# Kernel tuning notes

Hardware: AMD Instinct MI355X
Metric: run time of the kernel (lower is better)

Reference implementation:

```python
import jax, jax.numpy as jnp
import numpy as np


def gcn_conv(x, edge_index, edge_weight, W, b):
    """Faithful PyG GCNConv: add self-loops (weight 1), symmetric normalization,
    linear transform, weighted sum aggregation at target nodes, then bias."""
    N = x.shape[0]
    loops = jnp.arange(N, dtype=edge_index.dtype)
    row = jnp.concatenate([edge_index[0], loops])  # source j
    col = jnp.concatenate([edge_index[1], loops])  # target i
    ew = jnp.concatenate([edge_weight, jnp.ones((N,), dtype=edge_weight.dtype)])
    deg = jax.ops.segment_sum(ew, col, num_segments=N)  # [N]
    dinv = jnp.where(deg > 0, jax.lax.rsqrt(deg), 0.0)
    norm = dinv[row] * ew * dinv[col]  # [E+N]
    xw = x @ W  # [N, F_out]
    msgs = xw[row] * norm[:, None]  # [E+N, F_out]
    out = jax.ops.segment_sum(msgs, col, num_segments=N)  # [N, F_out]
    return out + b


def setup_inputs() -> dict:
    key = jax.random.key(0)
    k = jax.random.split(key, 8)
    N, E, Fin, Fhid, Fout = 50000, 800000, 128, 128, 64
    x = jax.random.normal(k[0], (N, Fin), dtype=jnp.float32)
    edge_index = jax.random.randint(k[1], (2, E), 0, N, dtype=jnp.int64)
    edge_weight = jax.random.uniform(k[2], (E,), dtype=jnp.float32)
    s0 = 1.0 / np.sqrt(Fin)
    s1 = 1.0 / np.sqrt(Fhid)
    W0 = jax.random.uniform(k[3], (Fin, Fhid), jnp.float32, -s0, s0)
    b0 = jnp.zeros((Fhid,), jnp.float32)
    W1 = jax.random.uniform(k[4], (Fhid, Fout), jnp.float32, -s1, s1)
    b1 = jnp.zeros((Fout,), jnp.float32)
    return {"x": x, "edge_index": edge_index, "edge_weight": edge_weight,
            "W0": W0, "b0": b0, "W1": W1, "b1": b1}


def reference(x, edge_index, edge_weight, W0, b0, W1, b1):
    # Encoder with num_layers=2, drop_p=0.0 (identity), activation=ReLU
    h = gcn_conv(x, edge_index, edge_weight, W0, b0)
    h = jax.nn.relu(h)
    h = gcn_conv(h, edge_index, edge_weight, W1, b1)
    h = jax.nn.relu(h)
    return h
```

## Files before the change

### kernel.cpp

```cpp
#include <hip/hip_runtime.h>

#define MAXDEG 48
#define BSH 6
#define BNODES 64
#define BCAP 2048

typedef unsigned short ushort_t;
typedef __attribute__((ext_vector_type(8))) short short8;
typedef __attribute__((ext_vector_type(4))) float f32x4;

__device__ inline ushort_t f2bf(float f) {
    union { float f; unsigned u; } v;
    v.f = f;
    unsigned r = v.u + 0x7fff + ((v.u >> 16) & 1);
    return (ushort_t)(r >> 16);
}

__device__ inline float bf2f_lo(unsigned u) {
    union { unsigned u; float f; } v;
    v.u = u << 16;
    return v.f;
}

__device__ inline float bf2f_hi(unsigned u) {
    union { unsigned u; float f; } v;
    v.u = u & 0xffff0000u;
    return v.f;
}


__global__ void k_setup(const float* __restrict__ W0, ushort_t* __restrict__ wp0,
                        const float* __restrict__ W1, ushort_t* __restrict__ wp1,
                        int* __restrict__ bcur, int NB) {
    int tid = blockIdx.x * blockDim.x + threadIdx.x;
    int stride = gridDim.x * blockDim.x;
    for (int i = tid; i < NB; i += stride) bcur[i] = 0;
    for (int e = tid; e < 16384; e += stride) {
        int j = e & 7, l = (e >> 3) & 63, ct = e >> 9;
        int t = ct & 7, c = ct >> 3;
        int k = 32 * c + (l >> 4) * 8 + j;
        int n = 16 * t + (l & 15);
        wp0[e] = f2bf(W0[k * 128 + n]);
    }
    for (int e = tid; e < 8192; e += stride) {
        int j = e & 7, l = (e >> 3) & 63, ct = e >> 9;
        int t = ct & 3, c = ct >> 2;
        int k = 32 * c + (l >> 4) * 8 + j;
        int n = 16 * t + (l & 15);
        wp1[e] = f2bf(W1[k * 64 + n]);
    }
}


__global__ __launch_bounds__(256) void k_scatter(const int* __restrict__ row,
                                                 const int* __restrict__ col,
                                                 const float* __restrict__ ew,
                                                 int* __restrict__ bcur,
                                                 uint2* __restrict__ recs, int E, int NB) {
    __shared__ int cnt[1024];
    __shared__ int base[1024];
    const int t = threadIdx.x;
    const size_t e0 = (size_t)blockIdx.x * 1024;
    for (int i = t; i < NB; i += 256) cnt[i] = 0;
    __syncthreads();
    int ck[4], rk[4];
#pragma unroll
    for (int j = 0; j < 4; ++j) {
        size_t e = e0 + (size_t)j * 256 + t;
        ck[j] = -1;
        if (e < (size_t)E) {
            int c = col[e];
            ck[j] = c;
            rk[j] = atomicAdd(&cnt[c >> BSH], 1);
        }
    }
    __syncthreads();
    for (int i = t; i < NB; i += 256) {
        int c = cnt[i];
        base[i] = c ? atomicAdd(&bcur[i], c) : 0;
    }
    __syncthreads();
#pragma unroll
    for (int j = 0; j < 4; ++j) {
        if (ck[j] >= 0) {
            size_t e = e0 + (size_t)j * 256 + t;
            int c = ck[j];
            int b = c >> BSH;
            int idx = base[b] + rk[j];
            if (idx < BCAP) {
                uint2 r;
                r.x = (unsigned)row[e] | ((unsigned)(c & (BNODES - 1)) << 16);
                r.y = __float_as_uint(ew[e]);
                recs[(size_t)b * BCAP + idx] = r;
            }
        }
    }
}


__global__ __launch_bounds__(256) void k_ell_build(const uint2* __restrict__ recs,
                                                   const int* __restrict__ bcur,
                                                   uint2* __restrict__ ell,
                                                   int* __restrict__ counts,
                                                   float* __restrict__ dinv, int N) {
    __shared__ uint2 tile[BNODES * MAXDEG];
    __shared__ int cnt[BNODES];
    const int b = blockIdx.x;
    const int t = threadIdx.x;
    if (t < BNODES) cnt[t] = 0;
    __syncthreads();
    const size_t s = (size_t)b * BCAP;
    const int ne = min(bcur[b], BCAP);
    for (int i = t; i < ne; i += 256) {
        uint2 r = recs[s + i];
        int dl = (r.x >> 16) & (BNODES - 1);
        int pos = atomicAdd(&cnt[dl], 1);
        if (pos < MAXDEG) {
            uint2 c;
            c.x = r.x & 0xffffu;
            c.y = r.y;
            tile[dl * MAXDEG + pos] = c;
        }
    }
    __syncthreads();
    const int node0 = b << BSH;
    if (t < BNODES) {
        int node = node0 + t;
        if (node < N) {
            int cn = min(cnt[t], MAXDEG);
            float sum = 1.0f;
            for (int j = 0; j < cn; ++j) sum += __uint_as_float(tile[t * MAXDEG + j].y);
            dinv[node] = rsqrtf(sum);
            counts[node] = cn;
        }
    }
    __syncthreads();
    const int nvalid = min(BNODES, N - node0);
    const int total = nvalid * MAXDEG;
    for (int i = t; i < total; i += 256) {
        int nl = i / MAXDEG;
        int slot = i - nl * MAXDEG;
        if (slot < min(cnt[nl], MAXDEG))
            ell[(size_t)node0 * MAXDEG + i] = tile[i];
    }
}


__global__ __launch_bounds__(256) void k_gemm1(const float* __restrict__ X,
                                               const uint4* __restrict__ Wp,
                                               ushort_t* __restrict__ Y, int N) {
    const int wave = threadIdx.x >> 6;
    const int lane = threadIdx.x & 63;
    const int m0 = blockIdx.x * 64 + wave * 16;
    if (m0 >= N) return;
    const int q = lane >> 4;
    const int mr = lane & 15;
    const int rowc = min(m0 + mr, N - 1);

    short8 a[4];
    const float* xr = X + (size_t)rowc * 128 + q * 8;
#pragma unroll
    for (int c = 0; c < 4; ++c) {
        float4 v0 = *(const float4*)(xr + 32 * c);
        float4 v1 = *(const float4*)(xr + 32 * c + 4);
        a[c][0] = (short)f2bf(v0.x); a[c][1] = (short)f2bf(v0.y);
        a[c][2] = (short)f2bf(v0.z); a[c][3] = (short)f2bf(v0.w);
        a[c][4] = (short)f2bf(v1.x); a[c][5] = (short)f2bf(v1.y);
        a[c][6] = (short)f2bf(v1.z); a[c][7] = (short)f2bf(v1.w);
    }

#pragma unroll
    for (int t = 0; t < 8; ++t) {
        f32x4 acc = {0.0f, 0.0f, 0.0f, 0.0f};
#pragma unroll
        for (int c = 0; c < 4; ++c) {
            uint4 bw = Wp[(size_t)(c * 8 + t) * 64 + lane];
            short8 b;
            __builtin_memcpy(&b, &bw, 16);
            acc = __builtin_amdgcn_mfma_f32_16x16x32_bf16(a[c], b, acc, 0, 0, 0);
        }
        const int colbase = 16 * t + mr;
#pragma unroll
        for (int r = 0; r < 4; ++r) {
            int orow = m0 + q * 4 + r;
            if (orow < N) Y[(size_t)orow * 128 + colbase] = f2bf(acc[r]);
        }
    }
}


__global__ __launch_bounds__(256) void k_gather128_gemm2(
        const int* __restrict__ counts, const uint2* __restrict__ ell,
        const float* __restrict__ dinv, const unsigned* __restrict__ xwb,
        const float* __restrict__ b0, const uint4* __restrict__ wp1,
        ushort_t* __restrict__ xw2b, int N) {
    __shared__ ushort_t h1[16][136];
    const int wave = threadIdx.x >> 6, lane = threadIdx.x & 63;
    const int node0 = blockIdx.x * 16;

#pragma unroll
    for (int k = 0; k < 4; ++k) {
        const int nl = wave * 4 + k;
        const int node = node0 + nl;
        unsigned packed = 0u;
        if (node < N) {
            float di = dinv[node];
            int cnt = min(counts[node], MAXDEG);
            int sv = 0;
            float wv = 0.0f;
            if (lane < cnt) {
                uint2 rec = ell[(size_t)node * MAXDEG + lane];
                sv = (int)rec.x;
                wv = dinv[sv] * __uint_as_float(rec.y) * di;
            }
            unsigned u0 = xwb[(size_t)node * 64 + lane];
            float2 bb = ((const float2*)b0)[lane];
            float sw = di * di;
            float ax = bb.x + bf2f_lo(u0) * sw;
            float ay = bb.y + bf2f_hi(u0) * sw;
            int j = 0;
            for (; j + 4 <= cnt; j += 4) {
                int s0 = __shfl(sv, j), s1 = __shfl(sv, j + 1),
                    s2 = __shfl(sv, j + 2), s3 = __shfl(sv, j + 3);
                float w0 = __shfl(wv, j), w1 = __shfl(wv, j + 1),
                      w2 = __shfl(wv, j + 2), w3 = __shfl(wv, j + 3);
                unsigned v0 = xwb[(size_t)s0 * 64 + lane];
                unsigned v1 = xwb[(size_t)s1 * 64 + lane];
                unsigned v2 = xwb[(size_t)s2 * 64 + lane];
                unsigned v3 = xwb[(size_t)s3 * 64 + lane];
                ax += bf2f_lo(v0) * w0; ay += bf2f_hi(v0) * w0;
                ax += bf2f_lo(v1) * w1; ay += bf2f_hi(v1) * w1;
                ax += bf2f_lo(v2) * w2; ay += bf2f_hi(v2) * w2;
                ax += bf2f_lo(v3) * w3; ay += bf2f_hi(v3) * w3;
            }
            for (; j < cnt; ++j) {
                int s = __shfl(sv, j);
                float w = __shfl(wv, j);
                unsigned v = xwb[(size_t)s * 64 + lane];
                ax += bf2f_lo(v) * w; ay += bf2f_hi(v) * w;
            }
            packed = ((unsigned)f2bf(fmaxf(ay, 0.0f)) << 16) | f2bf(fmaxf(ax, 0.0f));
        }
        *(unsigned*)&h1[nl][2 * lane] = packed;
    }
    __syncthreads();

    const int q = lane >> 4, mr = lane & 15;
    short8 a[4];
#pragma unroll
    for (int c = 0; c < 4; ++c)
        __builtin_memcpy(&a[c], &h1[mr][32 * c + 8 * q], 16);
    f32x4 acc = {0.0f, 0.0f, 0.0f, 0.0f};
#pragma unroll
    for (int c = 0; c < 4; ++c) {
        uint4 bw = wp1[(size_t)(c * 4 + wave) * 64 + lane];
        short8 bf;
        __builtin_memcpy(&bf, &bw, 16);
        acc = __builtin_amdgcn_mfma_f32_16x16x32_bf16(a[c], bf, acc, 0, 0, 0);
    }
    const int colb = 16 * wave + mr;
#pragma unroll
    for (int r = 0; r < 4; ++r) {
        int orow = node0 + q * 4 + r;
        if (orow < N) xw2b[(size_t)orow * 64 + colb] = f2bf(acc[r]);
    }
}


__global__ __launch_bounds__(256) void k_gather64_relu(const int* __restrict__ counts,
                                                       const uint2* __restrict__ ell,
                                                       const float* __restrict__ dinv,
                                                       const ushort_t* __restrict__ xwb,
                                                       const float* __restrict__ bias,
                                                       float* __restrict__ h, int N) {
    int node = (blockIdx.x * 256 + threadIdx.x) >> 6;
    int lane = threadIdx.x & 63;
    if (node >= N) return;
    float di = dinv[node];
    int cnt = min(counts[node], MAXDEG);

    int sv = 0;
    float wv = 0.0f;
    if (lane < cnt) {
        uint2 rec = ell[(size_t)node * MAXDEG + lane];
        sv = (int)rec.x;
        wv = dinv[sv] * __uint_as_float(rec.y) * di;
    }

    float acc = bias[lane] + bf2f_lo((unsigned)xwb[(size_t)node * 64 + lane]) * di * di;

    int j = 0;
    for (; j + 4 <= cnt; j += 4) {
        int s0 = __shfl(sv, j), s1 = __shfl(sv, j + 1), s2 = __shfl(sv, j + 2), s3 = __shfl(sv, j + 3);
        float w0 = __shfl(wv, j), w1 = __shfl(wv, j + 1), w2 = __shfl(wv, j + 2), w3 = __shfl(wv, j + 3);
        float v0 = bf2f_lo((unsigned)xwb[(size_t)s0 * 64 + lane]);
        float v1 = bf2f_lo((unsigned)xwb[(size_t)s1 * 64 + lane]);
        float v2 = bf2f_lo((unsigned)xwb[(size_t)s2 * 64 + lane]);
        float v3 = bf2f_lo((unsigned)xwb[(size_t)s3 * 64 + lane]);
        acc += v0 * w0 + v1 * w1 + v2 * w2 + v3 * w3;
    }
    for (; j < cnt; ++j) {
        acc += bf2f_lo((unsigned)xwb[(size_t)__shfl(sv, j) * 64 + lane]) * __shfl(wv, j);
    }
    h[(size_t)node * 64 + lane] = fmaxf(acc, 0.0f);
}


extern "C" void kernel_launch(void* const* d_in, const int* in_sizes, int n_in,
                              void* d_out, int out_size, void* d_ws, size_t ws_size,
                              hipStream_t stream) {
    const float* x  = (const float*)d_in[0];
    const int*   ei = (const int*)d_in[1];
    const float* ew = (const float*)d_in[2];
    const float* W0 = (const float*)d_in[3];
    const float* b0 = (const float*)d_in[4];
    const float* W1 = (const float*)d_in[5];
    const float* b1 = (const float*)d_in[6];
    float* out = (float*)d_out;

    const int Fhid = in_sizes[4];
    const int Fin  = in_sizes[3] / Fhid;
    const int N    = in_sizes[0] / Fin;
    const int E    = in_sizes[2];
    const int NB   = (N + BNODES - 1) >> BSH;

    const int* row = ei;
    const int* col = ei + E;

    char* w = (char*)d_ws;
    auto alloc = [&](size_t bytes) {
        char* p = w;
        w += (bytes + 255) & ~(size_t)255;
        return p;
    };
    float*    dinv   = (float*)alloc((size_t)N * 4);
    int*      counts = (int*)alloc((size_t)N * 4);
    int*      bcur   = (int*)alloc((size_t)NB * 4);
    uint2*    recs   = (uint2*)alloc((size_t)NB * BCAP * 8);
    uint2*    ell    = (uint2*)alloc((size_t)N * MAXDEG * 8);
    ushort_t* xw1b   = (ushort_t*)alloc((size_t)N * 128 * 2);
    ushort_t* xw2b   = (ushort_t*)alloc((size_t)N * 64 * 2);
    ushort_t* wp0    = (ushort_t*)alloc(16384 * 2);
    ushort_t* wp1    = (ushort_t*)alloc(8192 * 2);

    const int T = 256;
    const int GB = (N + 63) / 64;

    k_setup<<<32, T, 0, stream>>>(W0, wp0, W1, wp1, bcur, NB);
    k_scatter<<<(E + 1023) / 1024, T, 0, stream>>>(row, col, ew, bcur, recs, E, NB);
    k_ell_build<<<NB, T, 0, stream>>>(recs, bcur, ell, counts, dinv, N);
    k_gemm1<<<GB, T, 0, stream>>>(x, (const uint4*)wp0, xw1b, N);
    k_gather128_gemm2<<<(N + 15) / 16, T, 0, stream>>>(counts, ell, dinv,
                                                       (const unsigned*)xw1b, b0,
                                                       (const uint4*)wp1, xw2b, N);
    k_gather64_relu<<<(N + 3) / 4, T, 0, stream>>>(counts, ell, dinv, xw2b, b1, out, N);
}
```

Before: 200.6 us.

## Build ELL with direct global atomics and fuse scatter with first GEMM

Replaces the two-pass bucketed scatter plus ELL build with a single pass that places each edge directly into the ELL slot using per-node global atomics, accumulating degree with float atomics. The dinv normalization is computed lazily via rsqrt of the degree inside the gather kernels. The scatter blocks are interleaved with the first GEMM blocks in one launch so both run concurrently. The gather128+GEMM2 kernel now handles 4 nodes per block for more parallelism, but wastes three quarters of its MFMA rows. Nondeterministic edge order and float atomic ordering change the rounding of results.

```diff
diff --git a/kernel.cpp b/kernel.cpp
--- a/kernel.cpp
+++ b/kernel.cpp
@@ -1,9 +1,6 @@
 #include <hip/hip_runtime.h>
 
 #define MAXDEG 48
-#define BSH 6
-#define BNODES 64
-#define BCAP 2048
 
 typedef unsigned short ushort_t;
 typedef __attribute__((ext_vector_type(8))) short short8;
@@ -29,12 +26,18 @@
 }
 
 
-__global__ void k_setup(const float* __restrict__ W0, ushort_t* __restrict__ wp0,
-                        const float* __restrict__ W1, ushort_t* __restrict__ wp1,
-                        int* __restrict__ bcur, int NB) {
+__global__ __launch_bounds__(256) void k_setup(const float* __restrict__ W0,
+                                               ushort_t* __restrict__ wp0,
+                                               const float* __restrict__ W1,
+                                               ushort_t* __restrict__ wp1,
+                                               int* __restrict__ counts,
+                                               float* __restrict__ deg, int N) {
     int tid = blockIdx.x * blockDim.x + threadIdx.x;
     int stride = gridDim.x * blockDim.x;
-    for (int i = tid; i < NB; i += stride) bcur[i] = 0;
+    for (int i = tid; i < N; i += stride) {
+        counts[i] = 0;
+        deg[i] = 0.0f;
+    }
     for (int e = tid; e < 16384; e += stride) {
         int j = e & 7, l = (e >> 3) & 63, ct = e >> 9;
         int t = ct & 7, c = ct >> 3;
@@ -52,106 +55,12 @@
 }
 
 
-__global__ __launch_bounds__(256) void k_scatter(const int* __restrict__ row,
-                                                 const int* __restrict__ col,
-                                                 const float* __restrict__ ew,
-                                                 int* __restrict__ bcur,
-                                                 uint2* __restrict__ recs, int E, int NB) {
-    __shared__ int cnt[1024];
-    __shared__ int base[1024];
-    const int t = threadIdx.x;
-    const size_t e0 = (size_t)blockIdx.x * 1024;
-    for (int i = t; i < NB; i += 256) cnt[i] = 0;
-    __syncthreads();
-    int ck[4], rk[4];
-#pragma unroll
-    for (int j = 0; j < 4; ++j) {
-        size_t e = e0 + (size_t)j * 256 + t;
-        ck[j] = -1;
-        if (e < (size_t)E) {
-            int c = col[e];
-            ck[j] = c;
-            rk[j] = atomicAdd(&cnt[c >> BSH], 1);
-        }
-    }
-    __syncthreads();
-    for (int i = t; i < NB; i += 256) {
-        int c = cnt[i];
-        base[i] = c ? atomicAdd(&bcur[i], c) : 0;
-    }
-    __syncthreads();
-#pragma unroll
-    for (int j = 0; j < 4; ++j) {
-        if (ck[j] >= 0) {
-            size_t e = e0 + (size_t)j * 256 + t;
-            int c = ck[j];
-            int b = c >> BSH;
-            int idx = base[b] + rk[j];
-            if (idx < BCAP) {
-                uint2 r;
-                r.x = (unsigned)row[e] | ((unsigned)(c & (BNODES - 1)) << 16);
-                r.y = __float_as_uint(ew[e]);
-                recs[(size_t)b * BCAP + idx] = r;
-            }
-        }
-    }
-}
-
-
-__global__ __launch_bounds__(256) void k_ell_build(const uint2* __restrict__ recs,
-                                                   const int* __restrict__ bcur,
-                                                   uint2* __restrict__ ell,
-                                                   int* __restrict__ counts,
-                                                   float* __restrict__ dinv, int N) {
-    __shared__ uint2 tile[BNODES * MAXDEG];
-    __shared__ int cnt[BNODES];
-    const int b = blockIdx.x;
-    const int t = threadIdx.x;
-    if (t < BNODES) cnt[t] = 0;
-    __syncthreads();
-    const size_t s = (size_t)b * BCAP;
-    const int ne = min(bcur[b], BCAP);
-    for (int i = t; i < ne; i += 256) {
-        uint2 r = recs[s + i];
-        int dl = (r.x >> 16) & (BNODES - 1);
-        int pos = atomicAdd(&cnt[dl], 1);
-        if (pos < MAXDEG) {
-            uint2 c;
-            c.x = r.x & 0xffffu;
-            c.y = r.y;
-            tile[dl * MAXDEG + pos] = c;
-        }
-    }
-    __syncthreads();
-    const int node0 = b << BSH;
-    if (t < BNODES) {
-        int node = node0 + t;
-        if (node < N) {
-            int cn = min(cnt[t], MAXDEG);
-            float sum = 1.0f;
-            for (int j = 0; j < cn; ++j) sum += __uint_as_float(tile[t * MAXDEG + j].y);
-            dinv[node] = rsqrtf(sum);
-            counts[node] = cn;
-        }
-    }
-    __syncthreads();
-    const int nvalid = min(BNODES, N - node0);
-    const int total = nvalid * MAXDEG;
-    for (int i = t; i < total; i += 256) {
-        int nl = i / MAXDEG;
-        int slot = i - nl * MAXDEG;
-        if (slot < min(cnt[nl], MAXDEG))
-            ell[(size_t)node0 * MAXDEG + i] = tile[i];
-    }
-}
-
-
-__global__ __launch_bounds__(256) void k_gemm1(const float* __restrict__ X,
-                                               const uint4* __restrict__ Wp,
-                                               ushort_t* __restrict__ Y, int N) {
+__device__ inline void gemm1_body(const float* __restrict__ X,
+                                  const uint4* __restrict__ Wp,
+                                  ushort_t* __restrict__ Y, int N, int g) {
     const int wave = threadIdx.x >> 6;
     const int lane = threadIdx.x & 63;
-    const int m0 = blockIdx.x * 64 + wave * 16;
+    const int m0 = g * 64 + wave * 16;
     if (m0 >= N) return;
     const int q = lane >> 4;
     const int mr = lane & 15;
@@ -189,67 +98,105 @@
 }
 
 
+__global__ __launch_bounds__(256) void k_scatter_gemm1(
+        const int* __restrict__ row, const int* __restrict__ col,
+        const float* __restrict__ ew, int* __restrict__ counts,
+        float* __restrict__ deg, uint2* __restrict__ ell, int E,
+        const float* __restrict__ x, const uint4* __restrict__ wp0,
+        ushort_t* __restrict__ xw1b, int N, int GB, int SB) {
+    const int bid = blockIdx.x;
+    const int npair = 2 * min(GB, SB);
+    bool isg;
+    int sub;
+    if (bid < npair) {
+        isg = (bid & 1) == 0;
+        sub = bid >> 1;
+    } else {
+        sub = min(GB, SB) + (bid - npair);
+        isg = GB > SB;
+    }
+    if (isg) {
+        gemm1_body(x, wp0, xw1b, N, sub);
+        return;
+    }
+    const int t = threadIdx.x;
+    const size_t e0 = (size_t)sub * 1024;
+#pragma unroll
+    for (int j = 0; j < 4; ++j) {
+        size_t e = e0 + (size_t)j * 256 + t;
+        if (e < (size_t)E) {
+            int c = col[e];
+            float w = ew[e];
+            int pos = atomicAdd(&counts[c], 1);
+            atomicAdd(&deg[c], w);
+            if (pos < MAXDEG) {
+                uint2 r;
+                r.x = (unsigned)row[e];
+                r.y = __float_as_uint(w);
+                ell[(size_t)c * MAXDEG + pos] = r;
+            }
+        }
+    }
+}
+
+
 __global__ __launch_bounds__(256) void k_gather128_gemm2(
         const int* __restrict__ counts, const uint2* __restrict__ ell,
-        const float* __restrict__ dinv, const unsigned* __restrict__ xwb,
+        const float* __restrict__ deg, const unsigned* __restrict__ xwb,
         const float* __restrict__ b0, const uint4* __restrict__ wp1,
         ushort_t* __restrict__ xw2b, int N) {
-    __shared__ ushort_t h1[16][136];
+    __shared__ ushort_t h1[4][136];
     const int wave = threadIdx.x >> 6, lane = threadIdx.x & 63;
-    const int node0 = blockIdx.x * 16;
-
-#pragma unroll
-    for (int k = 0; k < 4; ++k) {
-        const int nl = wave * 4 + k;
-        const int node = node0 + nl;
-        unsigned packed = 0u;
-        if (node < N) {
-            float di = dinv[node];
-            int cnt = min(counts[node], MAXDEG);
-            int sv = 0;
-            float wv = 0.0f;
-            if (lane < cnt) {
-                uint2 rec = ell[(size_t)node * MAXDEG + lane];
-                sv = (int)rec.x;
-                wv = dinv[sv] * __uint_as_float(rec.y) * di;
-            }
-            unsigned u0 = xwb[(size_t)node * 64 + lane];
-            float2 bb = ((const float2*)b0)[lane];
-            float sw = di * di;
-            float ax = bb.x + bf2f_lo(u0) * sw;
-            float ay = bb.y + bf2f_hi(u0) * sw;
-            int j = 0;
-            for (; j + 4 <= cnt; j += 4) {
-                int s0 = __shfl(sv, j), s1 = __shfl(sv, j + 1),
-                    s2 = __shfl(sv, j + 2), s3 = __shfl(sv, j + 3);
-                float w0 = __shfl(wv, j), w1 = __shfl(wv, j + 1),
-                      w2 = __shfl(wv, j + 2), w3 = __shfl(wv, j + 3);
-                unsigned v0 = xwb[(size_t)s0 * 64 + lane];
-                unsigned v1 = xwb[(size_t)s1 * 64 + lane];
-                unsigned v2 = xwb[(size_t)s2 * 64 + lane];
-                unsigned v3 = xwb[(size_t)s3 * 64 + lane];
-                ax += bf2f_lo(v0) * w0; ay += bf2f_hi(v0) * w0;
-                ax += bf2f_lo(v1) * w1; ay += bf2f_hi(v1) * w1;
-                ax += bf2f_lo(v2) * w2; ay += bf2f_hi(v2) * w2;
-                ax += bf2f_lo(v3) * w3; ay += bf2f_hi(v3) * w3;
-            }
-            for (; j < cnt; ++j) {
-                int s = __shfl(sv, j);
-                float w = __shfl(wv, j);
-                unsigned v = xwb[(size_t)s * 64 + lane];
-                ax += bf2f_lo(v) * w; ay += bf2f_hi(v) * w;
-            }
-            packed = ((unsigned)f2bf(fmaxf(ay, 0.0f)) << 16) | f2bf(fmaxf(ax, 0.0f));
-        }
-        *(unsigned*)&h1[nl][2 * lane] = packed;
-    }
+    const int node0 = blockIdx.x * 4;
+    const int node = node0 + wave;
+
+    unsigned packed = 0u;
+    if (node < N) {
+        float di = rsqrtf(deg[node] + 1.0f);
+        int cnt = min(counts[node], MAXDEG);
+        int sv = 0;
+        float wv = 0.0f;
+        if (lane < cnt) {
+            uint2 rec = ell[(size_t)node * MAXDEG + lane];
+            sv = (int)rec.x;
+            wv = rsqrtf(deg[sv] + 1.0f) * __uint_as_float(rec.y) * di;
+        }
+        unsigned u0 = xwb[(size_t)node * 64 + lane];
+        float2 bb = ((const float2*)b0)[lane];
+        float sw = di * di;
+        float ax = bb.x + bf2f_lo(u0) * sw;
+        float ay = bb.y + bf2f_hi(u0) * sw;
+        int j = 0;
+        for (; j + 4 <= cnt; j += 4) {
+            int s0 = __shfl(sv, j), s1 = __shfl(sv, j + 1),
+                s2 = __shfl(sv, j + 2), s3 = __shfl(sv, j + 3);
+            float w0 = __shfl(wv, j), w1 = __shfl(wv, j + 1),
+                  w2 = __shfl(wv, j + 2), w3 = __shfl(wv, j + 3);
+            unsigned v0 = xwb[(size_t)s0 * 64 + lane];
+            unsigned v1 = xwb[(size_t)s1 * 64 + lane];
+            unsigned v2 = xwb[(size_t)s2 * 64 + lane];
+            unsigned v3 = xwb[(size_t)s3 * 64 + lane];
+            ax += bf2f_lo(v0) * w0; ay += bf2f_hi(v0) * w0;
+            ax += bf2f_lo(v1) * w1; ay += bf2f_hi(v1) * w1;
+            ax += bf2f_lo(v2) * w2; ay += bf2f_hi(v2) * w2;
+            ax += bf2f_lo(v3) * w3; ay += bf2f_hi(v3) * w3;
+        }
+        for (; j < cnt; ++j) {
+            int s = __shfl(sv, j);
+            float w = __shfl(wv, j);
+            unsigned v = xwb[(size_t)s * 64 + lane];
+            ax += bf2f_lo(v) * w; ay += bf2f_hi(v) * w;
+        }
+        packed = ((unsigned)f2bf(fmaxf(ay, 0.0f)) << 16) | f2bf(fmaxf(ax, 0.0f));
+    }
+    *(unsigned*)&h1[wave][2 * lane] = packed;
     __syncthreads();
 
     const int q = lane >> 4, mr = lane & 15;
     short8 a[4];
 #pragma unroll
     for (int c = 0; c < 4; ++c)
-        __builtin_memcpy(&a[c], &h1[mr][32 * c + 8 * q], 16);
+        __builtin_memcpy(&a[c], &h1[mr & 3][32 * c + 8 * q], 16);
     f32x4 acc = {0.0f, 0.0f, 0.0f, 0.0f};
 #pragma unroll
     for (int c = 0; c < 4; ++c) {
@@ -258,25 +205,26 @@
         __builtin_memcpy(&bf, &bw, 16);
         acc = __builtin_amdgcn_mfma_f32_16x16x32_bf16(a[c], bf, acc, 0, 0, 0);
     }
-    const int colb = 16 * wave + mr;
-#pragma unroll
-    for (int r = 0; r < 4; ++r) {
-        int orow = node0 + q * 4 + r;
-        if (orow < N) xw2b[(size_t)orow * 64 + colb] = f2bf(acc[r]);
+    if (q == 0) {
+#pragma unroll
+        for (int r = 0; r < 4; ++r) {
+            int orow = node0 + r;
+            if (orow < N) xw2b[(size_t)orow * 64 + 16 * wave + mr] = f2bf(acc[r]);
+        }
     }
 }
 
 
 __global__ __launch_bounds__(256) void k_gather64_relu(const int* __restrict__ counts,
                                                        const uint2* __restrict__ ell,
-                                                       const float* __restrict__ dinv,
+                                                       const float* __restrict__ deg,
                                                        const ushort_t* __restrict__ xwb,
                                                        const float* __restrict__ bias,
                                                        float* __restrict__ h, int N) {
     int node = (blockIdx.x * 256 + threadIdx.x) >> 6;
     int lane = threadIdx.x & 63;
     if (node >= N) return;
-    float di = dinv[node];
+    float di = rsqrtf(deg[node] + 1.0f);
     int cnt = min(counts[node], MAXDEG);
 
     int sv = 0;
@@ -284,7 +232,7 @@
     if (lane < cnt) {
         uint2 rec = ell[(size_t)node * MAXDEG + lane];
         sv = (int)rec.x;
-        wv = dinv[sv] * __uint_as_float(rec.y) * di;
+        wv = rsqrtf(deg[sv] + 1.0f) * __uint_as_float(rec.y) * di;
     }
 
     float acc = bias[lane] + bf2f_lo((unsigned)xwb[(size_t)node * 64 + lane]) * di * di;
@@ -322,7 +270,6 @@
     const int Fin  = in_sizes[3] / Fhid;
     const int N    = in_sizes[0] / Fin;
     const int E    = in_sizes[2];
-    const int NB   = (N + BNODES - 1) >> BSH;
 
     const int* row = ei;
     const int* col = ei + E;
@@ -333,10 +280,8 @@
         w += (bytes + 255) & ~(size_t)255;
         return p;
     };
-    float*    dinv   = (float*)alloc((size_t)N * 4);
+    float*    deg    = (float*)alloc((size_t)N * 4);
     int*      counts = (int*)alloc((size_t)N * 4);
-    int*      bcur   = (int*)alloc((size_t)NB * 4);
-    uint2*    recs   = (uint2*)alloc((size_t)NB * BCAP * 8);
     uint2*    ell    = (uint2*)alloc((size_t)N * MAXDEG * 8);
     ushort_t* xw1b   = (ushort_t*)alloc((size_t)N * 128 * 2);
     ushort_t* xw2b   = (ushort_t*)alloc((size_t)N * 64 * 2);
@@ -345,13 +290,13 @@
 
     const int T = 256;
     const int GB = (N + 63) / 64;
-
-    k_setup<<<32, T, 0, stream>>>(W0, wp0, W1, wp1, bcur, NB);
-    k_scatter<<<(E + 1023) / 1024, T, 0, stream>>>(row, col, ew, bcur, recs, E, NB);
-    k_ell_build<<<NB, T, 0, stream>>>(recs, bcur, ell, counts, dinv, N);
-    k_gemm1<<<GB, T, 0, stream>>>(x, (const uint4*)wp0, xw1b, N);
-    k_gather128_gemm2<<<(N + 15) / 16, T, 0, stream>>>(counts, ell, dinv,
-                                                       (const unsigned*)xw1b, b0,
-                                                       (const uint4*)wp1, xw2b, N);
-    k_gather64_relu<<<(N + 3) / 4, T, 0, stream>>>(counts, ell, dinv, xw2b, b1, out, N);
-}
+    const int SB = (E + 1023) / 1024;
+
+    k_setup<<<96, T, 0, stream>>>(W0, wp0, W1, wp1, counts, deg, N);
+    k_scatter_gemm1<<<GB + SB, T, 0, stream>>>(row, col, ew, counts, deg, ell, E,
+                                               x, (const uint4*)wp0, xw1b, N, GB, SB);
+    k_gather128_gemm2<<<(N + 3) / 4, T, 0, stream>>>(counts, ell, deg,
+                                                     (const unsigned*)xw1b, b0,
+                                                     (const uint4*)wp1, xw2b, N);
+    k_gather64_relu<<<(N + 3) / 4, T, 0, stream>>>(counts, ell, deg, xw2b, b1, out, N);
+}
```

Result: slower. 231.5 us (+15.4%).
